# Optimization experiments

Measured on AMD Instinct MI355X. Metric: run time of the kernel, lower is better.

## Reference

```python
import jax, jax.numpy as jnp
import numpy as np

NOISE_LEVEL = 0.05  # midpoint of uniform(0.01, 0.1) in the original
A_COEF = 0.99
B_COEF = 0.01


def setup_inputs() -> dict:
    key = jax.random.key(0)
    k1, k2 = jax.random.split(key)
    C, T = 256, 220500
    waveform = jax.random.normal(k1, (C, T), dtype=jnp.float32)
    white_noise = jax.random.normal(k2, (C, T), dtype=jnp.float32)
    return {"waveform": waveform, "white_noise": white_noise}


def _pink_noise(white_noise):
    # First-order IIR: f[0] = w[0]; f[i] = 0.99*f[i-1] + 0.01*w[i]
    # Vectorized over channels, lax.scan over time.
    w0 = white_noise[:, 0]                      # [C]
    wt = white_noise[:, 1:].T                   # [T-1, C]

    def step(carry, w_t):
        f = A_COEF * carry + B_COEF * w_t
        return f, f

    _, rest = jax.lax.scan(step, w0, wt)        # rest: [T-1, C]
    pink = jnp.concatenate([w0[None, :], rest], axis=0).T  # [C, T]
    return pink


def reference(waveform, white_noise):
    pink = _pink_noise(white_noise)
    mixed = waveform + pink * NOISE_LEVEL
    max_val = jnp.max(jnp.abs(mixed))
    # normalize only if peak exceeds 1.0
    return jnp.where(max_val > 1.0, mixed / max_val, mixed)
```

## Files before the change

### kernel.cpp

```cpp
#include <hip/hip_runtime.h>


#define TLEN 220500
#define CHANNELS 256

constexpr int SEGL = 2048;
constexpr int WUP  = 512;
constexpr int SPC  = (TLEN + SEGL - 1) / SEGL;
constexpr int NSEG = SPC * CHANNELS;
constexpr int NBLOCKS = 2048;
constexpr int GRID_WAVES = NBLOCKS * 4;

constexpr float AC = 0.99f;
constexpr float BC = 0.01f;
constexpr float NL = 0.05f;

constexpr double dpow(double a, long n) { double r = 1.0; for (long i = 0; i < n; ++i) r *= a; return r; }

constexpr float S8P0 = (float)dpow(0.99, 8);
constexpr float S8P1 = (float)dpow(0.99, 16);
constexpr float S8P2 = (float)dpow(0.99, 32);
constexpr float S8P3 = (float)dpow(0.99, 64);
constexpr float S8P4 = (float)dpow(0.99, 128);
constexpr float S8P5 = (float)dpow(0.99, 256);
constexpr float A512 = (float)dpow(0.99, 512);
constexpr float L2A8 = -0.11599655756609923f;

typedef float f4 __attribute__((ext_vector_type(4)));

__device__ __forceinline__ f4 ntld4(const float* p) {
    return __builtin_nontemporal_load(reinterpret_cast<const f4*>(p));
}

__device__ __forceinline__ float wave_scan8(float f, int lane) {
    { float o = __shfl_up(f, 1,  64); if (lane >= 1)  f = fmaf(S8P0, o, f); }
    { float o = __shfl_up(f, 2,  64); if (lane >= 2)  f = fmaf(S8P1, o, f); }
    { float o = __shfl_up(f, 4,  64); if (lane >= 4)  f = fmaf(S8P2, o, f); }
    { float o = __shfl_up(f, 8,  64); if (lane >= 8)  f = fmaf(S8P3, o, f); }
    { float o = __shfl_up(f, 16, 64); if (lane >= 16) f = fmaf(S8P4, o, f); }
    { float o = __shfl_up(f, 32, 64); if (lane >= 32) f = fmaf(S8P5, o, f); }
    return f;
}

__device__ __forceinline__ float serial8(const f4& a, const f4& b) {
    float f = BC * a.x;
    f = fmaf(AC, f, BC * a.y);
    f = fmaf(AC, f, BC * a.z);
    f = fmaf(AC, f, BC * a.w);
    f = fmaf(AC, f, BC * b.x);
    f = fmaf(AC, f, BC * b.y);
    f = fmaf(AC, f, BC * b.z);
    f = fmaf(AC, f, BC * b.w);
    return f;
}

__global__ void init_max_kernel(unsigned int* gmax) { *gmax = 0u; }

template <int USE_ATOMIC>
__global__ __launch_bounds__(256)
void fused_kernel(const float* __restrict__ waveform,
                  const float* __restrict__ white,
                  float* __restrict__ out,
                  unsigned int* __restrict__ gmax,
                  float* __restrict__ blockmax)
{
    __shared__ float sM[4];
    const int tid  = threadIdx.x;
    const int lane = tid & 63;
    const int wv   = tid >> 6;
    const int l8   = 8 * lane;
    const float D8L = __builtin_exp2f((float)lane * L2A8);
    const f4 z4 = {0.f, 0.f, 0.f, 0.f};

    float mx = 0.f;

    for (int S = blockIdx.x * 4 + wv; S < NSEG; S += GRID_WAVES) {
        const int ch = S / SPC;
        const int s  = S - ch * SPC;
        const size_t row = (size_t)ch * TLEN;
        const float* __restrict__ wrow = white + row;
        const float* __restrict__ arow = waveform + row;
        float* __restrict__ orow = out + row;
        const int seg0 = s * SEGL;

        f4 wu0 = z4, wu1 = z4;
        if (s > 0) {
            const float* wb = wrow + (seg0 - WUP) + l8;
            wu0 = ntld4(wb);
            wu1 = ntld4(wb + 4);
        }
        f4 Wa[4], Wb[4], Aa[4], Ab[4];
        #pragma unroll
        for (int p = 0; p < 4; ++p) {
            const int g = seg0 + p * 512 + l8;
            Wa[p] = z4; Wb[p] = z4; Aa[p] = z4; Ab[p] = z4;
            if (g < TLEN) {
                Wa[p] = ntld4(wrow + g);
                Aa[p] = ntld4(arow + g);
            }
            if (g + 4 < TLEN) {
                Wb[p] = ntld4(wrow + g + 4);
                Ab[p] = ntld4(arow + g + 4);
            }
        }

        float Tw = 0.f;
        if (s > 0) {
            float f = serial8(wu0, wu1);
            float p = wave_scan8(f, lane);
            Tw = __shfl(p, 63, 64);
        }
        float eB[4], T[4];
        #pragma unroll
        for (int p = 0; p < 4; ++p) {
            float f  = serial8(Wa[p], Wb[p]);
            float sc = wave_scan8(f, lane);
            float ex = __shfl_up(sc, 1, 64);
            eB[p] = (lane == 0) ? 0.f : ex;
            T[p]  = __shfl(sc, 63, 64);
        }

        float E = (s > 0) ? Tw : __shfl(Wa[0].x, 0, 64);

        #pragma unroll
        for (int p = 0; p < 4; ++p) {
            float f = fmaf(D8L, E, eB[p]);
            f4 ma, mb;
            f = fmaf(AC, f, BC * Wa[p].x); ma.x = fmaf(NL, f, Aa[p].x);
            f = fmaf(AC, f, BC * Wa[p].y); ma.y = fmaf(NL, f, Aa[p].y);
            f = fmaf(AC, f, BC * Wa[p].z); ma.z = fmaf(NL, f, Aa[p].z);
            f = fmaf(AC, f, BC * Wa[p].w); ma.w = fmaf(NL, f, Aa[p].w);
            f = fmaf(AC, f, BC * Wb[p].x); mb.x = fmaf(NL, f, Ab[p].x);
            f = fmaf(AC, f, BC * Wb[p].y); mb.y = fmaf(NL, f, Ab[p].y);
            f = fmaf(AC, f, BC * Wb[p].z); mb.z = fmaf(NL, f, Ab[p].z);
            f = fmaf(AC, f, BC * Wb[p].w); mb.w = fmaf(NL, f, Ab[p].w);

            const int g = seg0 + p * 512 + l8;
            if (g < TLEN) {
                *reinterpret_cast<f4*>(orow + g) = ma;
                mx = fmaxf(mx, fmaxf(fmaxf(fabsf(ma.x), fabsf(ma.y)),
                                     fmaxf(fabsf(ma.z), fabsf(ma.w))));
            }
            if (g + 4 < TLEN) {
                *reinterpret_cast<f4*>(orow + g + 4) = mb;
                mx = fmaxf(mx, fmaxf(fmaxf(fabsf(mb.x), fabsf(mb.y)),
                                     fmaxf(fabsf(mb.z), fabsf(mb.w))));
            }
            E = fmaf(A512, E, T[p]);
        }
    }

    #pragma unroll
    for (int d = 32; d >= 1; d >>= 1)
        mx = fmaxf(mx, __shfl_xor(mx, d, 64));
    if (lane == 0) sM[wv] = mx;
    __syncthreads();
    if (tid == 0) {
        float m = fmaxf(fmaxf(sM[0], sM[1]), fmaxf(sM[2], sM[3]));
        if (USE_ATOMIC) {
            atomicMax(gmax, __float_as_uint(m));
        } else {
            blockmax[blockIdx.x] = m;
        }
    }
}

__global__ __launch_bounds__(256)
void reduce_max_kernel(const float* __restrict__ blockmax, unsigned int* __restrict__ gmax)
{
    __shared__ float sM[4];
    const int tid  = threadIdx.x;
    const int lane = tid & 63;
    const int wv   = tid >> 6;
    float mx = 0.f;
    for (int i = tid; i < NBLOCKS; i += 256)
        mx = fmaxf(mx, blockmax[i]);
    #pragma unroll
    for (int d = 32; d >= 1; d >>= 1)
        mx = fmaxf(mx, __shfl_xor(mx, d, 64));
    if (lane == 0) sM[wv] = mx;
    __syncthreads();
    if (tid == 0)
        *gmax = __float_as_uint(fmaxf(fmaxf(sM[0], sM[1]), fmaxf(sM[2], sM[3])));
}

__global__ __launch_bounds__(256)
void scale_kernel(float* __restrict__ out, const unsigned int* __restrict__ gmax, int n4)
{
    const float m = __uint_as_float(*gmax);
    const float s = (m > 1.0f) ? (1.0f / m) : 1.0f;
    f4* p = reinterpret_cast<f4*>(out);
    int i = blockIdx.x * blockDim.x + threadIdx.x;
    const int stride = gridDim.x * blockDim.x;
    for (; i < n4; i += stride) {
        f4 v = p[i];
        v.x *= s; v.y *= s; v.z *= s; v.w *= s;
        __builtin_nontemporal_store(v, &p[i]);
    }
}

extern "C" void kernel_launch(void* const* d_in, const int* in_sizes, int n_in,
                              void* d_out, int out_size, void* d_ws, size_t ws_size,
                              hipStream_t stream)
{
    const float* waveform = (const float*)d_in[0];
    const float* white    = (const float*)d_in[1];
    float* out            = (float*)d_out;

    unsigned int* gmax = (unsigned int*)d_ws;
    float* blockmax    = (float*)((char*)d_ws + 256);
    const bool ws_ok   = ws_size >= 256 + (size_t)NBLOCKS * sizeof(float);

    const int n4 = out_size / 4;

    if (ws_ok) {
        hipLaunchKernelGGL((fused_kernel<0>), dim3(NBLOCKS), dim3(256), 0, stream,
                           waveform, white, out, gmax, blockmax);
        hipLaunchKernelGGL(reduce_max_kernel, dim3(1), dim3(256), 0, stream,
                           blockmax, gmax);
    } else {
        hipLaunchKernelGGL(init_max_kernel, dim3(1), dim3(1), 0, stream, gmax);
        hipLaunchKernelGGL((fused_kernel<1>), dim3(NBLOCKS), dim3(256), 0, stream,
                           waveform, white, out, gmax, blockmax);
    }
    hipLaunchKernelGGL(scale_kernel, dim3(3072), dim3(256), 0, stream,
                       out, gmax, n4);
}
```

Baseline: 232.8 us.

## Stream sub-blocks one at a time and use butterfly reduction for warm-up carry

Restructures the per-segment loop so each 512-sample sub-block is loaded, scanned and written before the next one, instead of loading all four sub-blocks into registers up front. This cuts register pressure, and a launch-bounds hint asks for 7 blocks per CU to raise occupancy. The warm-up carry now uses a weighted xor-shuffle sum instead of a full prefix scan plus broadcast. The cost is less memory-level parallelism per wave, since loads for later sub-blocks are no longer issued ahead of the compute.

```diff
diff --git a/kernel.cpp b/kernel.cpp
--- a/kernel.cpp
+++ b/kernel.cpp
@@ -5,6 +5,7 @@
 #define CHANNELS 256
 
 constexpr int SEGL = 2048;
+constexpr int SUB  = 512;
 constexpr int WUP  = 512;
 constexpr int SPC  = (TLEN + SEGL - 1) / SEGL;
 constexpr int NSEG = SPC * CHANNELS;
@@ -57,7 +58,7 @@
 __global__ void init_max_kernel(unsigned int* gmax) { *gmax = 0u; }
 
 template <int USE_ATOMIC>
-__global__ __launch_bounds__(256)
+__global__ __launch_bounds__(256, 7)
 void fused_kernel(const float* __restrict__ waveform,
                   const float* __restrict__ white,
                   float* __restrict__ out,
@@ -70,6 +71,7 @@
     const int wv   = tid >> 6;
     const int l8   = 8 * lane;
     const float D8L = __builtin_exp2f((float)lane * L2A8);
+    const float WSC = __builtin_exp2f((float)(63 - lane) * L2A8);
     const f4 z4 = {0.f, 0.f, 0.f, 0.f};
 
     float mx = 0.f;
@@ -83,70 +85,60 @@
         float* __restrict__ orow = out + row;
         const int seg0 = s * SEGL;
 
-        f4 wu0 = z4, wu1 = z4;
+        float E;
         if (s > 0) {
             const float* wb = wrow + (seg0 - WUP) + l8;
-            wu0 = ntld4(wb);
-            wu1 = ntld4(wb + 4);
+            f4 u0 = ntld4(wb);
+            f4 u1 = ntld4(wb + 4);
+            float fw = serial8(u0, u1) * WSC;
+            #pragma unroll
+            for (int d = 32; d >= 1; d >>= 1)
+                fw += __shfl_xor(fw, d, 64);
+            E = fw;
+        } else {
+            E = wrow[0];
         }
-        f4 Wa[4], Wb[4], Aa[4], Ab[4];
+
         #pragma unroll
-        for (int p = 0; p < 4; ++p) {
-            const int g = seg0 + p * 512 + l8;
-            Wa[p] = z4; Wb[p] = z4; Aa[p] = z4; Ab[p] = z4;
+        for (int k = 0; k < 4; ++k) {
+            const int g = seg0 + k * SUB + l8;
+            f4 W0 = z4, W1 = z4, A0 = z4, A1 = z4;
             if (g < TLEN) {
-                Wa[p] = ntld4(wrow + g);
-                Aa[p] = ntld4(arow + g);
+                W0 = ntld4(wrow + g);
+                A0 = ntld4(arow + g);
             }
             if (g + 4 < TLEN) {
-                Wb[p] = ntld4(wrow + g + 4);
-                Ab[p] = ntld4(arow + g + 4);
-            }
-        }
-
-        float Tw = 0.f;
-        if (s > 0) {
-            float f = serial8(wu0, wu1);
-            float p = wave_scan8(f, lane);
-            Tw = __shfl(p, 63, 64);
-        }
-        float eB[4], T[4];
-        #pragma unroll
-        for (int p = 0; p < 4; ++p) {
-            float f  = serial8(Wa[p], Wb[p]);
-            float sc = wave_scan8(f, lane);
-            float ex = __shfl_up(sc, 1, 64);
-            eB[p] = (lane == 0) ? 0.f : ex;
-            T[p]  = __shfl(sc, 63, 64);
-        }
-
-        float E = (s > 0) ? Tw : __shfl(Wa[0].x, 0, 64);
-
-        #pragma unroll
-        for (int p = 0; p < 4; ++p) {
-            float f = fmaf(D8L, E, eB[p]);
-            f4 ma, mb;
-            f = fmaf(AC, f, BC * Wa[p].x); ma.x = fmaf(NL, f, Aa[p].x);
-            f = fmaf(AC, f, BC * Wa[p].y); ma.y = fmaf(NL, f, Aa[p].y);
-            f = fmaf(AC, f, BC * Wa[p].z); ma.z = fmaf(NL, f, Aa[p].z);
-            f = fmaf(AC, f, BC * Wa[p].w); ma.w = fmaf(NL, f, Aa[p].w);
-            f = fmaf(AC, f, BC * Wb[p].x); mb.x = fmaf(NL, f, Ab[p].x);
-            f = fmaf(AC, f, BC * Wb[p].y); mb.y = fmaf(NL, f, Ab[p].y);
-            f = fmaf(AC, f, BC * Wb[p].z); mb.z = fmaf(NL, f, Ab[p].z);
-            f = fmaf(AC, f, BC * Wb[p].w); mb.w = fmaf(NL, f, Ab[p].w);
-
-            const int g = seg0 + p * 512 + l8;
+                W1 = ntld4(wrow + g + 4);
+                A1 = ntld4(arow + g + 4);
+            }
+            float f  = serial8(W0, W1);
+            float p  = wave_scan8(f, lane);
+            float e  = __shfl_up(p, 1, 64);
+            if (lane == 0) e = 0.f;
+            const float T = __shfl(p, 63, 64);
+
+            f = fmaf(D8L, E, e);
+            f4 m0, m1;
+            f = fmaf(AC, f, BC * W0.x); m0.x = fmaf(NL, f, A0.x);
+            f = fmaf(AC, f, BC * W0.y); m0.y = fmaf(NL, f, A0.y);
+            f = fmaf(AC, f, BC * W0.z); m0.z = fmaf(NL, f, A0.z);
+            f = fmaf(AC, f, BC * W0.w); m0.w = fmaf(NL, f, A0.w);
+            f = fmaf(AC, f, BC * W1.x); m1.x = fmaf(NL, f, A1.x);
+            f = fmaf(AC, f, BC * W1.y); m1.y = fmaf(NL, f, A1.y);
+            f = fmaf(AC, f, BC * W1.z); m1.z = fmaf(NL, f, A1.z);
+            f = fmaf(AC, f, BC * W1.w); m1.w = fmaf(NL, f, A1.w);
+
             if (g < TLEN) {
-                *reinterpret_cast<f4*>(orow + g) = ma;
-                mx = fmaxf(mx, fmaxf(fmaxf(fabsf(ma.x), fabsf(ma.y)),
-                                     fmaxf(fabsf(ma.z), fabsf(ma.w))));
+                *reinterpret_cast<f4*>(orow + g) = m0;
+                mx = fmaxf(mx, fmaxf(fmaxf(fabsf(m0.x), fabsf(m0.y)),
+                                     fmaxf(fabsf(m0.z), fabsf(m0.w))));
             }
             if (g + 4 < TLEN) {
-                *reinterpret_cast<f4*>(orow + g + 4) = mb;
-                mx = fmaxf(mx, fmaxf(fmaxf(fabsf(mb.x), fabsf(mb.y)),
-                                     fmaxf(fabsf(mb.z), fabsf(mb.w))));
-            }
-            E = fmaf(A512, E, T[p]);
+                *reinterpret_cast<f4*>(orow + g + 4) = m1;
+                mx = fmaxf(mx, fmaxf(fmaxf(fabsf(m1.x), fabsf(m1.y)),
+                                     fmaxf(fabsf(m1.z), fabsf(m1.w))));
+            }
+            E = fmaf(A512, E, T);
         }
     }
 
```

Result: slower. 241.6 us (+3.8%).
